# Kernel optimization log

Measured on AMD Instinct MI355X. Metric: run time of the kernel, lower is better.

## Reference

```python
import jax, jax.numpy as jnp
import numpy as np

NUM_EXPERTS = 16
HIDDEN = 2048
INTER = 1408  # moe_intermediate_size
TOKENS = 32768  # tokens pre-sorted by expert assignment
INIT_STD = 0.01  # flax nn.initializers.normal() default stddev


def setup_inputs() -> dict:
    key = jax.random.key(0)
    kx, kg, ku, kd = jax.random.split(key, 4)
    hidden_states = jax.random.normal(kx, (TOKENS, HIDDEN), jnp.float32)
    w_gate = jax.random.normal(kg, (NUM_EXPERTS, HIDDEN, INTER), jnp.float32) * INIT_STD
    w_up = jax.random.normal(ku, (NUM_EXPERTS, HIDDEN, INTER), jnp.float32) * INIT_STD
    w_down = jax.random.normal(kd, (NUM_EXPERTS, INTER, HIDDEN), jnp.float32) * INIT_STD
    # equal token assignment per expert; must sum to TOKENS
    group_sizes = jnp.full((NUM_EXPERTS,), TOKENS // NUM_EXPERTS, dtype=jnp.int32)
    return {
        "hidden_states": hidden_states,
        "w_gate": w_gate,
        "w_up": w_up,
        "w_down": w_down,
        "group_sizes": group_sizes,
    }


def reference(hidden_states, w_gate, w_up, w_down, group_sizes):
    # Grouped GEMM over experts: tokens [T,H] are sorted by expert;
    # group_sizes[e] tokens are multiplied by expert e's kernel.
    gate = jax.lax.ragged_dot(hidden_states, w_gate, group_sizes)  # [T, INTER]
    up = jax.lax.ragged_dot(hidden_states, w_up, group_sizes)      # [T, INTER]
    h = jax.nn.silu(gate) * up                                     # SwiGLU
    out = jax.lax.ragged_dot(h, w_down, group_sizes)               # [T, HIDDEN]
    return out
```

## Files before the change

### kernel.cpp

```cpp
#include <hip/hip_runtime.h>
#include <hip/hip_bf16.h>
#include <stdint.h>

#define TOKENS 32768
#define HIDDEN 2048
#define INTER  1408
#define NEXP   16

typedef unsigned short u16;
typedef __bf16 bf16x8  __attribute__((ext_vector_type(8)));
typedef float  floatx16 __attribute__((ext_vector_type(16)));

#define GLOAD_LDS(g, l) __builtin_amdgcn_global_load_lds( \
    (const __attribute__((address_space(1))) void*)(g),    \
    (__attribute__((address_space(3))) void*)(l), 16, 0, 0)

__device__ __forceinline__ u16 f2bf(float f) {
    uint32_t u = __builtin_bit_cast(uint32_t, f);
    u = (u + 0x7FFFu + ((u >> 16) & 1u)) >> 16;
    return (u16)u;
}

__global__ void convert_x(const float* __restrict__ src, u16* __restrict__ dst) {
    int idx = blockIdx.x * blockDim.x + threadIdx.x;
    float4 v = ((const float4*)src)[idx];
    ushort4 o;
    o.x = f2bf(v.x); o.y = f2bf(v.y); o.z = f2bf(v.z); o.w = f2bf(v.w);
    ((ushort4*)dst)[idx] = o;
}

__global__ void transpose_cvt(const float* __restrict__ src, u16* __restrict__ dst,
                              int R, int C) {
    __shared__ float tile[32][33];
    const int e  = blockIdx.z;
    const float* s = src + (size_t)e * R * C;
    u16*         d = dst + (size_t)e * R * C;
    const int r0 = blockIdx.y * 32, c0 = blockIdx.x * 32;
    const int tid = threadIdx.x;
#pragma unroll
    for (int p = 0; p < 4; ++p) {
        int t = p * 256 + tid;
        int sr = t >> 5, sc = t & 31;
        tile[sr][sc] = s[(size_t)(r0 + sr) * C + (c0 + sc)];
    }
    __syncthreads();
#pragma unroll
    for (int p = 0; p < 4; ++p) {
        int t = p * 256 + tid;
        int dr = t >> 5, dc = t & 31;
        d[(size_t)(c0 + dr) * R + (r0 + dc)] = f2bf(tile[dc][dr]);
    }
}

__global__ __launch_bounds__(256, 2)
void gemm_gateup(const u16* __restrict__ xb, const u16* __restrict__ wgb,
                 const u16* __restrict__ wub, const int* __restrict__ gsz,
                 u16* __restrict__ hbuf) {
    __shared__ __align__(16) u16 As[128 * 32];
    __shared__ __align__(16) u16 Bgs[128 * 32];
    __shared__ __align__(16) u16 Bus[128 * 32];

    const int tid  = threadIdx.x;
    const int wave = tid >> 6;
    const int lane = tid & 63;
    const int row0 = blockIdx.y * 128;
    const int col0 = blockIdx.x * 128;

    int e = 0, cum = 0;
    for (int i = 0; i < NEXP; ++i) {
        int s = gsz[i];
        if (row0 >= cum + s) cum += s; else { e = i; break; }
    }

    const int seg0 = wave * 128 + lane;
    const int seg1 = seg0 + 64;
    const int m0 = seg0 >> 2, k80 = (seg0 & 3) * 8;
    const int m1 = seg1 >> 2, k81 = (seg1 & 3) * 8;

    const u16* pA0 = xb + (size_t)(row0 + m0) * HIDDEN + k80;
    const u16* pA1 = xb + (size_t)(row0 + m1) * HIDDEN + k81;
    const size_t wb = (size_t)e * INTER + col0;
    const u16* pG0 = wgb + (wb + m0) * HIDDEN + k80;
    const u16* pG1 = wgb + (wb + m1) * HIDDEN + k81;
    const u16* pU0 = wub + (wb + m0) * HIDDEN + k80;
    const u16* pU1 = wub + (wb + m1) * HIDDEN + k81;

    u16* lA0 = As  + (size_t)(wave * 128) * 8;   u16* lA1 = lA0 + 64 * 8;
    u16* lG0 = Bgs + (size_t)(wave * 128) * 8;   u16* lG1 = lG0 + 64 * 8;
    u16* lU0 = Bus + (size_t)(wave * 128) * 8;   u16* lU1 = lU0 + 64 * 8;

    const int wm = (wave >> 1) * 64;
    const int wn = (wave & 1) * 64;
    const int lm = lane & 31;
    const int lk = (lane >> 5) * 8;

    floatx16 zero;
#pragma unroll
    for (int i = 0; i < 16; ++i) zero[i] = 0.f;
    floatx16 ag[2][2], au[2][2];
#pragma unroll
    for (int i = 0; i < 2; ++i)
#pragma unroll
        for (int j = 0; j < 2; ++j) { ag[i][j] = zero; au[i][j] = zero; }

    for (int it = 0; it < HIDDEN / 32; ++it) {
        GLOAD_LDS(pA0, lA0); GLOAD_LDS(pA1, lA1);
        GLOAD_LDS(pG0, lG0); GLOAD_LDS(pG1, lG1);
        GLOAD_LDS(pU0, lU0); GLOAD_LDS(pU1, lU1);
        __syncthreads();
#pragma unroll
        for (int ks = 0; ks < 2; ++ks) {
            const int ko = ks * 16 + lk;
            bf16x8 a[2], bg[2], bu[2];
#pragma unroll
            for (int i = 0; i < 2; ++i) {
                a[i]  = *(const bf16x8*)(As  + (wm + i * 32 + lm) * 32 + ko);
                bg[i] = *(const bf16x8*)(Bgs + (wn + i * 32 + lm) * 32 + ko);
                bu[i] = *(const bf16x8*)(Bus + (wn + i * 32 + lm) * 32 + ko);
            }
#pragma unroll
            for (int i = 0; i < 2; ++i)
#pragma unroll
                for (int j = 0; j < 2; ++j) {
                    ag[i][j] = __builtin_amdgcn_mfma_f32_32x32x16_bf16(a[i], bg[j], ag[i][j], 0, 0, 0);
                    au[i][j] = __builtin_amdgcn_mfma_f32_32x32x16_bf16(a[i], bu[j], au[i][j], 0, 0, 0);
                }
        }
        __syncthreads();
        pA0 += 32; pA1 += 32; pG0 += 32; pG1 += 32; pU0 += 32; pU1 += 32;
    }

    const int rb = 4 * (lane >> 5);
#pragma unroll
    for (int i = 0; i < 2; ++i)
#pragma unroll
        for (int j = 0; j < 2; ++j)
#pragma unroll
            for (int r = 0; r < 16; ++r) {
                int rr = wm + i * 32 + rb + (r & 3) + 8 * (r >> 2);
                int cc = wn + j * 32 + lm;
                float g = ag[i][j][r], u = au[i][j][r];
                float h = (g / (1.f + __expf(-g))) * u;
                hbuf[(size_t)(row0 + rr) * INTER + (col0 + cc)] = f2bf(h);
            }
}

__global__ __launch_bounds__(256, 2)
void gemm_down(const u16* __restrict__ hbuf, const u16* __restrict__ wdb,
               const int* __restrict__ gsz, float* __restrict__ out) {
    __shared__ __align__(16) u16 As[128 * 32];
    __shared__ __align__(16) u16 Bs[128 * 32];

    const int tid  = threadIdx.x;
    const int wave = tid >> 6;
    const int lane = tid & 63;
    const int row0 = blockIdx.y * 128;
    const int col0 = blockIdx.x * 128;

    int e = 0, cum = 0;
    for (int i = 0; i < NEXP; ++i) {
        int s = gsz[i];
        if (row0 >= cum + s) cum += s; else { e = i; break; }
    }

    const int seg0 = wave * 128 + lane;
    const int seg1 = seg0 + 64;
    const int m0 = seg0 >> 2, k80 = (seg0 & 3) * 8;
    const int m1 = seg1 >> 2, k81 = (seg1 & 3) * 8;

    const u16* pA0 = hbuf + (size_t)(row0 + m0) * INTER + k80;
    const u16* pA1 = hbuf + (size_t)(row0 + m1) * INTER + k81;
    const size_t wb = (size_t)e * HIDDEN + col0;
    const u16* pB0 = wdb + (wb + m0) * INTER + k80;
    const u16* pB1 = wdb + (wb + m1) * INTER + k81;

    u16* lA0 = As + (size_t)(wave * 128) * 8;  u16* lA1 = lA0 + 64 * 8;
    u16* lB0 = Bs + (size_t)(wave * 128) * 8;  u16* lB1 = lB0 + 64 * 8;

    const int wm = (wave >> 1) * 64;
    const int wn = (wave & 1) * 64;
    const int lm = lane & 31;
    const int lk = (lane >> 5) * 8;

    floatx16 zero;
#pragma unroll
    for (int i = 0; i < 16; ++i) zero[i] = 0.f;
    floatx16 ac[2][2];
#pragma unroll
    for (int i = 0; i < 2; ++i)
#pragma unroll
        for (int j = 0; j < 2; ++j) ac[i][j] = zero;

    for (int it = 0; it < INTER / 32; ++it) {
        GLOAD_LDS(pA0, lA0); GLOAD_LDS(pA1, lA1);
        GLOAD_LDS(pB0, lB0); GLOAD_LDS(pB1, lB1);
        __syncthreads();
#pragma unroll
        for (int ks = 0; ks < 2; ++ks) {
            const int ko = ks * 16 + lk;
            bf16x8 a[2], b[2];
#pragma unroll
            for (int i = 0; i < 2; ++i) {
                a[i] = *(const bf16x8*)(As + (wm + i * 32 + lm) * 32 + ko);
                b[i] = *(const bf16x8*)(Bs + (wn + i * 32 + lm) * 32 + ko);
            }
#pragma unroll
            for (int i = 0; i < 2; ++i)
#pragma unroll
                for (int j = 0; j < 2; ++j)
                    ac[i][j] = __builtin_amdgcn_mfma_f32_32x32x16_bf16(a[i], b[j], ac[i][j], 0, 0, 0);
        }
        __syncthreads();
        pA0 += 32; pA1 += 32; pB0 += 32; pB1 += 32;
    }

    const int rb = 4 * (lane >> 5);
#pragma unroll
    for (int i = 0; i < 2; ++i)
#pragma unroll
        for (int j = 0; j < 2; ++j)
#pragma unroll
            for (int r = 0; r < 16; ++r) {
                int rr = wm + i * 32 + rb + (r & 3) + 8 * (r >> 2);
                int cc = wn + j * 32 + lm;
                out[(size_t)(row0 + rr) * HIDDEN + (col0 + cc)] = ac[i][j][r];
            }
}

extern "C" void kernel_launch(void* const* d_in, const int* in_sizes, int n_in,
                              void* d_out, int out_size, void* d_ws, size_t ws_size,
                              hipStream_t stream) {
    const float* x  = (const float*)d_in[0];
    const float* wg = (const float*)d_in[1];
    const float* wu = (const float*)d_in[2];
    const float* wd = (const float*)d_in[3];
    const int*  gsz = (const int*)d_in[4];
    float* out = (float*)d_out;

    const size_t XB_BYTES = (size_t)TOKENS * HIDDEN * 2;
    const size_t W_BYTES  = (size_t)NEXP * HIDDEN * INTER * 2;
    char* ws = (char*)d_ws;
    u16* xb   = (u16*)(ws);
    u16* wgb  = (u16*)(ws + XB_BYTES);
    u16* wub  = (u16*)(ws + XB_BYTES + W_BYTES);
    u16* wdb  = (u16*)(ws + XB_BYTES + 2 * W_BYTES);
    u16* hbuf = (u16*)(ws + XB_BYTES + 3 * W_BYTES);

    convert_x<<<(TOKENS * HIDDEN) / (4 * 256), 256, 0, stream>>>(x, xb);

    dim3 tg(INTER / 32, HIDDEN / 32, NEXP);
    transpose_cvt<<<tg, 256, 0, stream>>>(wg, wgb, HIDDEN, INTER);
    transpose_cvt<<<tg, 256, 0, stream>>>(wu, wub, HIDDEN, INTER);
    dim3 td(HIDDEN / 32, INTER / 32, NEXP);
    transpose_cvt<<<td, 256, 0, stream>>>(wd, wdb, INTER, HIDDEN);

    gemm_gateup<<<dim3(INTER / 128, TOKENS / 128), 256, 0, stream>>>(xb, wgb, wub, gsz, hbuf);
    gemm_down<<<dim3(HIDDEN / 128, TOKENS / 128), 256, 0, stream>>>(hbuf, wdb, gsz, out);
}
```

Before: 1.588 ms.

## Double-buffer GEMM LDS, swizzle layout, XCD-aware tile mapping, vectorized transpose

Both grouped GEMM kernels now double-buffer their LDS tiles so the next K-slice's global-to-LDS loads overlap the current slice's MFMAs. LDS columns are XOR-swizzled to reduce bank conflicts on the fragment reads. Blocks are remapped so consecutive tiles on the same XCD share row panels, which should improve L2 reuse. The weight transpose/convert kernel moves to 64x64 tiles with float4 reads and 16-byte bf16 writes. LDS use doubles, which may lower occupancy.

```diff
diff --git a/kernel.cpp b/kernel.cpp
--- a/kernel.cpp
+++ b/kernel.cpp
@@ -1,5 +1,4 @@
 #include <hip/hip_runtime.h>
-#include <hip/hip_bf16.h>
 #include <stdint.h>
 
 #define TOKENS 32768
@@ -10,6 +9,7 @@
 typedef unsigned short u16;
 typedef __bf16 bf16x8  __attribute__((ext_vector_type(8)));
 typedef float  floatx16 __attribute__((ext_vector_type(16)));
+typedef unsigned short u16x8 __attribute__((ext_vector_type(8)));
 
 #define GLOAD_LDS(g, l) __builtin_amdgcn_global_load_lds( \
     (const __attribute__((address_space(1))) void*)(g),    \
@@ -31,24 +31,34 @@
 
 __global__ void transpose_cvt(const float* __restrict__ src, u16* __restrict__ dst,
                               int R, int C) {
-    __shared__ float tile[32][33];
+    __shared__ __align__(16) u16 tl[64][72];
     const int e  = blockIdx.z;
     const float* s = src + (size_t)e * R * C;
     u16*         d = dst + (size_t)e * R * C;
-    const int r0 = blockIdx.y * 32, c0 = blockIdx.x * 32;
+    const int r0 = blockIdx.y * 64, c0 = blockIdx.x * 64;
     const int tid = threadIdx.x;
-#pragma unroll
-    for (int p = 0; p < 4; ++p) {
-        int t = p * 256 + tid;
-        int sr = t >> 5, sc = t & 31;
-        tile[sr][sc] = s[(size_t)(r0 + sr) * C + (c0 + sc)];
+    const int c4 = (tid & 15) * 4;
+    const int rq = tid >> 4;
+    float m[4][4];
+#pragma unroll
+    for (int k = 0; k < 4; ++k) {
+        float4 v = *(const float4*)(s + (size_t)(r0 + rq * 4 + k) * C + (c0 + c4));
+        m[k][0] = v.x; m[k][1] = v.y; m[k][2] = v.z; m[k][3] = v.w;
+    }
+#pragma unroll
+    for (int j = 0; j < 4; ++j) {
+        ushort4 o;
+        o.x = f2bf(m[0][j]); o.y = f2bf(m[1][j]); o.z = f2bf(m[2][j]); o.w = f2bf(m[3][j]);
+        *(ushort4*)&tl[c4 + j][rq * 4] = o;
     }
     __syncthreads();
 #pragma unroll
-    for (int p = 0; p < 4; ++p) {
-        int t = p * 256 + tid;
-        int dr = t >> 5, dc = t & 31;
-        d[(size_t)(c0 + dr) * R + (r0 + dc)] = f2bf(tile[dc][dr]);
+    for (int p = 0; p < 2; ++p) {
+        int q  = p * 256 + tid;
+        int oc = q >> 3;
+        int r8 = (q & 7) * 8;
+        u16x8 w = *(const u16x8*)&tl[oc][r8];
+        *(u16x8*)(d + (size_t)(c0 + oc) * R + (r0 + r8)) = w;
     }
 }
 
@@ -56,81 +66,104 @@
 void gemm_gateup(const u16* __restrict__ xb, const u16* __restrict__ wgb,
                  const u16* __restrict__ wub, const int* __restrict__ gsz,
                  u16* __restrict__ hbuf) {
-    __shared__ __align__(16) u16 As[128 * 32];
-    __shared__ __align__(16) u16 Bgs[128 * 32];
-    __shared__ __align__(16) u16 Bus[128 * 32];
+    __shared__ __align__(16) u16 smem[2 * 3 * 128 * 32];
 
     const int tid  = threadIdx.x;
     const int wave = tid >> 6;
     const int lane = tid & 63;
-    const int row0 = blockIdx.y * 128;
-    const int col0 = blockIdx.x * 128;
+
+    const int id  = blockIdx.x;
+    const int xcd = id & 7;
+    const int t   = id >> 3;
+    const int sub = t / 88;
+    const int rem = t - sub * 88;
+    const int yc  = rem >> 3;
+    const int r8  = rem & 7;
+    const int row0 = (xcd * 32 + sub * 8 + r8) * 128;
+    const int col0 = yc * 128;
 
     int e = 0, cum = 0;
     for (int i = 0; i < NEXP; ++i) {
-        int s = gsz[i];
-        if (row0 >= cum + s) cum += s; else { e = i; break; }
-    }
-
-    const int seg0 = wave * 128 + lane;
-    const int seg1 = seg0 + 64;
-    const int m0 = seg0 >> 2, k80 = (seg0 & 3) * 8;
-    const int m1 = seg1 >> 2, k81 = (seg1 & 3) * 8;
-
-    const u16* pA0 = xb + (size_t)(row0 + m0) * HIDDEN + k80;
-    const u16* pA1 = xb + (size_t)(row0 + m1) * HIDDEN + k81;
+        int sgl = gsz[i];
+        if (row0 >= cum + sgl) cum += sgl; else { e = i; break; }
+    }
+
+    const int s0 = wave * 128 + lane;
+    const int m0 = s0 >> 2;
+    const int m1 = m0 + 16;
+    const int ck = (s0 & 3) ^ ((m0 >> 1) & 3);
+    const int ka = ck * 8;
+
+    const u16* pA0 = xb + (size_t)(row0 + m0) * HIDDEN + ka;
+    const u16* pA1 = xb + (size_t)(row0 + m1) * HIDDEN + ka;
     const size_t wb = (size_t)e * INTER + col0;
-    const u16* pG0 = wgb + (wb + m0) * HIDDEN + k80;
-    const u16* pG1 = wgb + (wb + m1) * HIDDEN + k81;
-    const u16* pU0 = wub + (wb + m0) * HIDDEN + k80;
-    const u16* pU1 = wub + (wb + m1) * HIDDEN + k81;
-
-    u16* lA0 = As  + (size_t)(wave * 128) * 8;   u16* lA1 = lA0 + 64 * 8;
-    u16* lG0 = Bgs + (size_t)(wave * 128) * 8;   u16* lG1 = lG0 + 64 * 8;
-    u16* lU0 = Bus + (size_t)(wave * 128) * 8;   u16* lU1 = lU0 + 64 * 8;
+    const u16* pG0 = wgb + (wb + m0) * HIDDEN + ka;
+    const u16* pG1 = wgb + (wb + m1) * HIDDEN + ka;
+    const u16* pU0 = wub + (wb + m0) * HIDDEN + ka;
+    const u16* pU1 = wub + (wb + m1) * HIDDEN + ka;
+
+    const int ldsW = wave * 1024;
 
     const int wm = (wave >> 1) * 64;
     const int wn = (wave & 1) * 64;
     const int lm = lane & 31;
-    const int lk = (lane >> 5) * 8;
-
-    floatx16 zero;
-#pragma unroll
-    for (int i = 0; i < 16; ++i) zero[i] = 0.f;
+    const int hi = lane >> 5;
+    const int key = (lm >> 1) & 3;
+    const int sw0 = ((0 + hi) ^ key) * 8;
+    const int sw1 = ((2 + hi) ^ key) * 8;
+
     floatx16 ag[2][2], au[2][2];
 #pragma unroll
     for (int i = 0; i < 2; ++i)
 #pragma unroll
-        for (int j = 0; j < 2; ++j) { ag[i][j] = zero; au[i][j] = zero; }
-
-    for (int it = 0; it < HIDDEN / 32; ++it) {
-        GLOAD_LDS(pA0, lA0); GLOAD_LDS(pA1, lA1);
-        GLOAD_LDS(pG0, lG0); GLOAD_LDS(pG1, lG1);
-        GLOAD_LDS(pU0, lU0); GLOAD_LDS(pU1, lU1);
+        for (int j = 0; j < 2; ++j)
+#pragma unroll
+            for (int r = 0; r < 16; ++r) { ag[i][j][r] = 0.f; au[i][j][r] = 0.f; }
+
+#define STAGE_GU(B) do { u16* _s = smem + (B) * 12288 + ldsW;                 \
+        GLOAD_LDS(pA0, _s);        GLOAD_LDS(pA1, _s + 512);                  \
+        GLOAD_LDS(pG0, _s + 4096); GLOAD_LDS(pG1, _s + 4608);                 \
+        GLOAD_LDS(pU0, _s + 8192); GLOAD_LDS(pU1, _s + 8704);                 \
+        pA0 += 32; pA1 += 32; pG0 += 32; pG1 += 32; pU0 += 32; pU1 += 32; } while (0)
+
+#define COMPUTE_GU(B) do {                                                    \
+        const u16* _A = smem + (B) * 12288;                                   \
+        const u16* _G = _A + 4096;                                            \
+        const u16* _U = _A + 8192;                                            \
+        _Pragma("unroll")                                                     \
+        for (int ks = 0; ks < 2; ++ks) {                                      \
+            const int sw = ks ? sw1 : sw0;                                    \
+            bf16x8 a[2], bg[2], bu[2];                                        \
+            _Pragma("unroll")                                                 \
+            for (int i = 0; i < 2; ++i) {                                     \
+                a[i]  = *(const bf16x8*)(_A + (wm + i * 32 + lm) * 32 + sw);  \
+                bg[i] = *(const bf16x8*)(_G + (wn + i * 32 + lm) * 32 + sw);  \
+                bu[i] = *(const bf16x8*)(_U + (wn + i * 32 + lm) * 32 + sw);  \
+            }                                                                 \
+            _Pragma("unroll")                                                 \
+            for (int i = 0; i < 2; ++i)                                       \
+                _Pragma("unroll")                                             \
+                for (int j = 0; j < 2; ++j) {                                 \
+                    ag[i][j] = __builtin_amdgcn_mfma_f32_32x32x16_bf16(a[i], bg[j], ag[i][j], 0, 0, 0); \
+                    au[i][j] = __builtin_amdgcn_mfma_f32_32x32x16_bf16(a[i], bu[j], au[i][j], 0, 0, 0); \
+                }                                                             \
+        } } while (0)
+
+    STAGE_GU(0);
+    __syncthreads();
+#pragma unroll 1
+    for (int it = 0; it < HIDDEN / 32; it += 2) {
+        STAGE_GU(1);
+        COMPUTE_GU(0);
         __syncthreads();
-#pragma unroll
-        for (int ks = 0; ks < 2; ++ks) {
-            const int ko = ks * 16 + lk;
-            bf16x8 a[2], bg[2], bu[2];
-#pragma unroll
-            for (int i = 0; i < 2; ++i) {
-                a[i]  = *(const bf16x8*)(As  + (wm + i * 32 + lm) * 32 + ko);
-                bg[i] = *(const bf16x8*)(Bgs + (wn + i * 32 + lm) * 32 + ko);
-                bu[i] = *(const bf16x8*)(Bus + (wn + i * 32 + lm) * 32 + ko);
-            }
-#pragma unroll
-            for (int i = 0; i < 2; ++i)
-#pragma unroll
-                for (int j = 0; j < 2; ++j) {
-                    ag[i][j] = __builtin_amdgcn_mfma_f32_32x32x16_bf16(a[i], bg[j], ag[i][j], 0, 0, 0);
-                    au[i][j] = __builtin_amdgcn_mfma_f32_32x32x16_bf16(a[i], bu[j], au[i][j], 0, 0, 0);
-                }
-        }
+        if (it + 2 < HIDDEN / 32) STAGE_GU(0);
+        COMPUTE_GU(1);
         __syncthreads();
-        pA0 += 32; pA1 += 32; pG0 += 32; pG1 += 32; pU0 += 32; pU1 += 32;
-    }
-
-    const int rb = 4 * (lane >> 5);
+    }
+#undef STAGE_GU
+#undef COMPUTE_GU
+
+    const int rb = 4 * hi;
 #pragma unroll
     for (int i = 0; i < 2; ++i)
 #pragma unroll
@@ -148,73 +181,97 @@
 __global__ __launch_bounds__(256, 2)
 void gemm_down(const u16* __restrict__ hbuf, const u16* __restrict__ wdb,
                const int* __restrict__ gsz, float* __restrict__ out) {
-    __shared__ __align__(16) u16 As[128 * 32];
-    __shared__ __align__(16) u16 Bs[128 * 32];
+    __shared__ __align__(16) u16 smem[2 * 2 * 128 * 32];
 
     const int tid  = threadIdx.x;
     const int wave = tid >> 6;
     const int lane = tid & 63;
-    const int row0 = blockIdx.y * 128;
-    const int col0 = blockIdx.x * 128;
+
+    const int id  = blockIdx.x;
+    const int xcd = id & 7;
+    const int t   = id >> 3;
+    const int sub = t >> 7;
+    const int rem = t & 127;
+    const int yc  = rem >> 3;
+    const int r8  = rem & 7;
+    const int row0 = (xcd * 32 + sub * 8 + r8) * 128;
+    const int col0 = yc * 128;
 
     int e = 0, cum = 0;
     for (int i = 0; i < NEXP; ++i) {
-        int s = gsz[i];
-        if (row0 >= cum + s) cum += s; else { e = i; break; }
-    }
-
-    const int seg0 = wave * 128 + lane;
-    const int seg1 = seg0 + 64;
-    const int m0 = seg0 >> 2, k80 = (seg0 & 3) * 8;
-    const int m1 = seg1 >> 2, k81 = (seg1 & 3) * 8;
-
-    const u16* pA0 = hbuf + (size_t)(row0 + m0) * INTER + k80;
-    const u16* pA1 = hbuf + (size_t)(row0 + m1) * INTER + k81;
+        int sgl = gsz[i];
+        if (row0 >= cum + sgl) cum += sgl; else { e = i; break; }
+    }
+
+    const int s0 = wave * 128 + lane;
+    const int m0 = s0 >> 2;
+    const int m1 = m0 + 16;
+    const int ck = (s0 & 3) ^ ((m0 >> 1) & 3);
+    const int ka = ck * 8;
+
+    const u16* pA0 = hbuf + (size_t)(row0 + m0) * INTER + ka;
+    const u16* pA1 = hbuf + (size_t)(row0 + m1) * INTER + ka;
     const size_t wb = (size_t)e * HIDDEN + col0;
-    const u16* pB0 = wdb + (wb + m0) * INTER + k80;
-    const u16* pB1 = wdb + (wb + m1) * INTER + k81;
-
-    u16* lA0 = As + (size_t)(wave * 128) * 8;  u16* lA1 = lA0 + 64 * 8;
-    u16* lB0 = Bs + (size_t)(wave * 128) * 8;  u16* lB1 = lB0 + 64 * 8;
+    const u16* pB0 = wdb + (wb + m0) * INTER + ka;
+    const u16* pB1 = wdb + (wb + m1) * INTER + ka;
+
+    const int ldsW = wave * 1024;
 
     const int wm = (wave >> 1) * 64;
     const int wn = (wave & 1) * 64;
     const int lm = lane & 31;
-    const int lk = (lane >> 5) * 8;
-
-    floatx16 zero;
-#pragma unroll
-    for (int i = 0; i < 16; ++i) zero[i] = 0.f;
+    const int hi = lane >> 5;
+    const int key = (lm >> 1) & 3;
+    const int sw0 = ((0 + hi) ^ key) * 8;
+    const int sw1 = ((2 + hi) ^ key) * 8;
+
     floatx16 ac[2][2];
 #pragma unroll
     for (int i = 0; i < 2; ++i)
 #pragma unroll
-        for (int j = 0; j < 2; ++j) ac[i][j] = zero;
-
-    for (int it = 0; it < INTER / 32; ++it) {
-        GLOAD_LDS(pA0, lA0); GLOAD_LDS(pA1, lA1);
-        GLOAD_LDS(pB0, lB0); GLOAD_LDS(pB1, lB1);
+        for (int j = 0; j < 2; ++j)
+#pragma unroll
+            for (int r = 0; r < 16; ++r) ac[i][j][r] = 0.f;
+
+#define STAGE_D(B) do { u16* _s = smem + (B) * 8192 + ldsW;                   \
+        GLOAD_LDS(pA0, _s);        GLOAD_LDS(pA1, _s + 512);                  \
+        GLOAD_LDS(pB0, _s + 4096); GLOAD_LDS(pB1, _s + 4608);                 \
+        pA0 += 32; pA1 += 32; pB0 += 32; pB1 += 32; } while (0)
+
+#define COMPUTE_D(B) do {                                                     \
+        const u16* _A = smem + (B) * 8192;                                    \
+        const u16* _B = _A + 4096;                                            \
+        _Pragma("unroll")                                                     \
+        for (int ks = 0; ks < 2; ++ks) {                                      \
+            const int sw = ks ? sw1 : sw0;                                    \
+            bf16x8 a[2], b[2];                                                \
+            _Pragma("unroll")                                                 \
+            for (int i = 0; i < 2; ++i) {                                     \
+                a[i] = *(const bf16x8*)(_A + (wm + i * 32 + lm) * 32 + sw);   \
+                b[i] = *(const bf16x8*)(_B + (wn + i * 32 + lm) * 32 + sw);   \
+            }                                                                 \
+            _Pragma("unroll")                                                 \
+            for (int i = 0; i < 2; ++i)                                       \
+                _Pragma("unroll")                                             \
+                for (int j = 0; j < 2; ++j)                                   \
+                    ac[i][j] = __builtin_amdgcn_mfma_f32_32x32x16_bf16(a[i], b[j], ac[i][j], 0, 0, 0); \
+        } } while (0)
+
+    STAGE_D(0);
+    __syncthreads();
+#pragma unroll 1
+    for (int it = 0; it < INTER / 32; it += 2) {
+        STAGE_D(1);
+        COMPUTE_D(0);
         __syncthreads();
-#pragma unroll
-        for (int ks = 0; ks < 2; ++ks) {
-            const int ko = ks * 16 + lk;
-            bf16x8 a[2], b[2];
-#pragma unroll
-            for (int i = 0; i < 2; ++i) {
-                a[i] = *(const bf16x8*)(As + (wm + i * 32 + lm) * 32 + ko);
-                b[i] = *(const bf16x8*)(Bs + (wn + i * 32 + lm) * 32 + ko);
-            }
-#pragma unroll
-            for (int i = 0; i < 2; ++i)
-#pragma unroll
-                for (int j = 0; j < 2; ++j)
-                    ac[i][j] = __builtin_amdgcn_mfma_f32_32x32x16_bf16(a[i], b[j], ac[i][j], 0, 0, 0);
-        }
+        if (it + 2 < INTER / 32) STAGE_D(0);
+        COMPUTE_D(1);
         __syncthreads();
-        pA0 += 32; pA1 += 32; pB0 += 32; pB1 += 32;
-    }
-
-    const int rb = 4 * (lane >> 5);
+    }
+#undef STAGE_D
+#undef COMPUTE_D
+
+    const int rb = 4 * hi;
 #pragma unroll
     for (int i = 0; i < 2; ++i)
 #pragma unroll
@@ -248,12 +305,12 @@
 
     convert_x<<<(TOKENS * HIDDEN) / (4 * 256), 256, 0, stream>>>(x, xb);
 
-    dim3 tg(INTER / 32, HIDDEN / 32, NEXP);
+    dim3 tg(INTER / 64, HIDDEN / 64, NEXP);
     transpose_cvt<<<tg, 256, 0, stream>>>(wg, wgb, HIDDEN, INTER);
     transpose_cvt<<<tg, 256, 0, stream>>>(wu, wub, HIDDEN, INTER);
-    dim3 td(HIDDEN / 32, INTER / 32, NEXP);
+    dim3 td(HIDDEN / 64, INTER / 64, NEXP);
     transpose_cvt<<<td, 256, 0, stream>>>(wd, wdb, INTER, HIDDEN);
 
-    gemm_gateup<<<dim3(INTER / 128, TOKENS / 128), 256, 0, stream>>>(xb, wgb, wub, gsz, hbuf);
-    gemm_down<<<dim3(HIDDEN / 128, TOKENS / 128), 256, 0, stream>>>(hbuf, wdb, gsz, out);
-}
+    gemm_gateup<<<256 * (INTER / 128), 256, 0, stream>>>(xb, wgb, wub, gsz, hbuf);
+    gemm_down<<<256 * (HIDDEN / 128), 256, 0, stream>>>(hbuf, wdb, gsz, out);
+}
```

Measured after the change: 1.439 ms. 1.1x faster.
